# Optimization experiments

Measured on AMD Instinct MI355X. Metric: run time of the kernel, lower is better.

Reference implementation:

```python
import jax, jax.numpy as jnp
import numpy as np

N, D, DIN, S, R = 128, 2560, 5120, 16, 160  # users, d_model, d_inner, d_state, dt_rank


def setup_inputs() -> dict:
    key = jax.random.key(0)
    ks = jax.random.split(key, 16)
    f = lambda k, shape, s: jax.random.normal(k, shape, dtype=jnp.float32) * s
    return {
        "x": f(ks[0], (1, 1, N, D), 1.0),
        "conv_state0": f(ks[1], (1, 1, N, DIN), 0.1),
        "conv_state1": f(ks[2], (1, 1, N, DIN), 0.1),
        "conv_state2": f(ks[3], (1, 1, N, DIN), 0.1),
        "conv_state3": f(ks[4], (1, 1, N, DIN), 0.1),
        "ssm_state": f(ks[5], (N, DIN, S), 0.1),
        "ssm_proj": f(ks[6], (D, DIN), 0.02),
        "mlp_proj": f(ks[7], (D, DIN), 0.02),
        "down_proj": f(ks[8], (DIN, D), 0.02),
        "conv_w": f(ks[9], (4, DIN), 0.2),
        "conv_bias": f(ks[10], (DIN,), 0.1),
        "x_proj_w": f(ks[11], (DIN, R + 2 * S), 0.02),
        "dt_proj_w": f(ks[12], (R, DIN), 0.05),
        "dt_proj_b": f(ks[13], (DIN,), 0.1),
        "A_log": jnp.log(jnp.broadcast_to(jnp.arange(1, S + 1, dtype=jnp.float32), (DIN, S))),
        "D_param": jnp.ones((DIN,), jnp.float32),
    }


def reference(x, conv_state0, conv_state1, conv_state2, conv_state3, ssm_state,
              ssm_proj, mlp_proj, down_proj, conv_w, conv_bias,
              x_proj_w, dt_proj_w, dt_proj_b, A_log, D_param):
    r = dt_proj_w.shape[0]
    s = A_log.shape[1]
    x2 = x[0, 0]                         # (N, D)
    xs = x2 @ ssm_proj                   # (N, DIN) in_proj (ssm half)
    # shifted conv state window: oldest state (conv_state0) is dropped
    states = (conv_state1[0, 0], conv_state2[0, 0], conv_state3[0, 0], xs)
    conv_out = conv_bias + conv_w[0] * states[0] + conv_w[1] * states[1] \
        + conv_w[2] * states[2] + conv_w[3] * states[3]   # (N, DIN)
    u = jax.nn.silu(conv_out)
    # selective-scan single step (TtMambaSSM)
    proj = u @ x_proj_w                  # (N, R + 2S)
    dt = jax.nn.softplus(proj[:, :r] @ dt_proj_w + dt_proj_b)  # (N, DIN)
    Bm = proj[:, r:r + s]                # (N, S)
    Cm = proj[:, r + s:]                 # (N, S)
    A = -jnp.exp(A_log)                  # (DIN, S)
    dA = jnp.exp(dt[:, :, None] * A[None])                     # (N, DIN, S)
    h = dA * ssm_state + dt[:, :, None] * Bm[:, None, :] * u[:, :, None]
    y = jnp.einsum('nds,ns->nd', h, Cm) + D_param * u          # (N, DIN)
    # residual/gate branch and output projection (note: no silu on res, as in source)
    res = x2 @ mlp_proj                  # (N, DIN)
    out = (y * res) @ down_proj          # (N, D)
    return out[None, None]               # (1, 1, N, D)
```

## Files before the change

kernel.cpp:

```cpp
#include <hip/hip_runtime.h>

using u16 = unsigned short;
using u32 = unsigned int;

typedef __attribute__((ext_vector_type(8))) short short8;
typedef __attribute__((ext_vector_type(4))) float floatx4;

constexpr int TOKENS = 128;
constexpr int DM = 2560;
constexpr int DI = 5120;
constexpr int NS = 16;
constexpr int NR = 160;
constexpr int NP = 192;

constexpr size_t ND    = (size_t)TOKENS * DI;
constexpr size_t XS_P  = 0;
constexpr size_t RES_P = XS_P + 5 * ND;
constexpr size_t U_OFF = RES_P + 5 * ND;
constexpr size_t DT_P  = U_OFF + ND;
constexpr size_t PRJ_P = DT_P + 5 * ND;
constexpr size_t PRJ   = PRJ_P + 40 * (size_t)(TOKENS * NP);
constexpr size_t NEED  = PRJ + (size_t)(TOKENS * NP);

constexpr size_t S_XS  = 0;
constexpr size_t S_RES = S_XS + ND;
constexpr size_t S_U   = S_RES + ND;
constexpr size_t S_DT  = S_U + ND;
constexpr size_t S_PRJ = S_DT + ND;
constexpr size_t S_OAC = S_PRJ + (size_t)(TOKENS * NP);

__device__ __forceinline__ float bf2f(u16 h) {
  u32 u = ((u32)h) << 16;
  return __builtin_bit_cast(float, u);
}
__device__ __forceinline__ u16 f2bf(float f) {
  u32 u = __builtin_bit_cast(u32, f);
  u += 0x7FFFu + ((u >> 16) & 1u);
  return (u16)(u >> 16);
}
__device__ __forceinline__ u32 pk2(float a, float b) {
  u32 r;
  asm("v_cvt_pk_bf16_f32 %0, %1, %2" : "=v"(r) : "v"(a), "v"(b));
  return r;
}
__device__ __forceinline__ uint4 pack8(uint4 lo, uint4 hi) {
  float4 a = __builtin_bit_cast(float4, lo), b = __builtin_bit_cast(float4, hi);
  return (uint4){pk2(a.x, a.y), pk2(a.z, a.w), pk2(b.x, b.y), pk2(b.z, b.w)};
}
__device__ __forceinline__ float ldsc(const void* p, size_t i, bool bf) {
  return bf ? bf2f(((const u16*)p)[i]) : ((const float*)p)[i];
}
__device__ __forceinline__ void ld8f(const void* p, size_t i, bool bf, float* o) {
  if (bf) {
    uint4 v = *(const uint4*)((const u16*)p + i);
    const u16* h = (const u16*)&v;
#pragma unroll
    for (int e = 0; e < 8; e++) o[e] = bf2f(h[e]);
  } else {
    const float4* f = (const float4*)((const float*)p + i);
    float4 a = f[0], b = f[1];
    o[0] = a.x; o[1] = a.y; o[2] = a.z; o[3] = a.w;
    o[4] = b.x; o[5] = b.y; o[6] = b.z; o[7] = b.w;
  }
}

struct GemmP {
  const void* A; int lda; int a_ws;
  const void* B; const void* B2;
  float* C; float* C2;
  int ldb; int ldc;
  int ksteps;
  int nx_half;
  int atomic;
  size_t cstride;
  const u32* probe;
};

__global__ __launch_bounds__(256, 3) void gemm_k(GemmP p) {
  __shared__ __align__(16) u16 As[2 * 128 * 32];
  __shared__ __align__(16) u16 Bs[2 * 64 * 32];

  const bool bf = (p.probe[0] != 0u);
  const int tid = threadIdx.x;
  const int bx = blockIdx.x;
  const void* B = p.B; float* C = p.C;
  int nblk = bx;
  if (bx >= p.nx_half) { B = p.B2; C = p.C2; nblk = bx - p.nx_half; }
  const int n0 = nblk * 64;
  const int kstart = blockIdx.y * p.ksteps * 32;
  if (!p.atomic) C += blockIdx.y * p.cstride;

  const int wave = tid >> 6, lane = tid & 63;
  const int q = lane >> 4, l16 = lane & 15;
  const int wx = wave & 1, wy = wave >> 1;

  const bool a_f32 = p.a_ws || !bf;

  const int ac = tid & 3;
  const int am0 = tid >> 2;
  const bool bact = tid < 128;
  const int bc = tid & 7, pr = (tid >> 3) & 15;
  const int bn8 = bc * 8, k2 = 2 * pr;

  floatx4 acc[4][2];
#pragma unroll
  for (int mi = 0; mi < 4; mi++)
#pragma unroll
    for (int ni = 0; ni < 2; ni++) acc[mi][ni] = (floatx4){0.f, 0.f, 0.f, 0.f};

  auto load_tiles = [&](int ks, uint4* ra, uint4* rb) {
    const int kb = kstart + ks * 32;
    if (!a_f32) {
      ra[0] = *(const uint4*)((const u16*)p.A + (size_t)am0 * p.lda + kb + ac * 8);
      ra[1] = *(const uint4*)((const u16*)p.A + (size_t)(am0 + 64) * p.lda + kb + ac * 8);
    } else {
      const float* Af = (const float*)p.A;
      const float4* f0 = (const float4*)(Af + (size_t)am0 * p.lda + kb + ac * 8);
      const float4* f1 = (const float4*)(Af + (size_t)(am0 + 64) * p.lda + kb + ac * 8);
      ra[0] = __builtin_bit_cast(uint4, f0[0]); ra[1] = __builtin_bit_cast(uint4, f0[1]);
      ra[2] = __builtin_bit_cast(uint4, f1[0]); ra[3] = __builtin_bit_cast(uint4, f1[1]);
    }
    if (bact) {
      if (bf) {
        rb[0] = *(const uint4*)((const u16*)B + (size_t)(kb + k2) * p.ldb + n0 + bn8);
        rb[1] = *(const uint4*)((const u16*)B + (size_t)(kb + k2 + 1) * p.ldb + n0 + bn8);
      } else {
        const float* Bf = (const float*)B;
        const float4* g0 = (const float4*)(Bf + (size_t)(kb + k2) * p.ldb + n0 + bn8);
        const float4* g1 = (const float4*)(Bf + (size_t)(kb + k2 + 1) * p.ldb + n0 + bn8);
        rb[0] = __builtin_bit_cast(uint4, g0[0]); rb[1] = __builtin_bit_cast(uint4, g0[1]);
        rb[2] = __builtin_bit_cast(uint4, g1[0]); rb[3] = __builtin_bit_cast(uint4, g1[1]);
      }
    }
  };

  auto store_tiles = [&](int b, const uint4* ra, const uint4* rb) {
    u16* Ab = &As[b * 4096];
    u16* Bb = &Bs[b * 2048];
    uint4 w0, w1;
    if (!a_f32) { w0 = ra[0]; w1 = ra[1]; }
    else        { w0 = pack8(ra[0], ra[1]); w1 = pack8(ra[2], ra[3]); }
    *(uint4*)&Ab[am0 * 32 + ((ac ^ (am0 & 3)) << 3)] = w0;
    const int m1 = am0 + 64;
    *(uint4*)&Ab[m1 * 32 + ((ac ^ (m1 & 3)) << 3)] = w1;
    if (bact) {
      u32 pk[8];
      if (bf) {
        const u16* lo = (const u16*)&rb[0];
        const u16* hi = (const u16*)&rb[1];
#pragma unroll
        for (int j = 0; j < 8; j++) pk[j] = (u32)lo[j] | ((u32)hi[j] << 16);
      } else {
        const float* lo = (const float*)&rb[0];
        const float* hi = (const float*)&rb[2];
#pragma unroll
        for (int j = 0; j < 8; j++) pk[j] = pk2(lo[j], hi[j]);
      }
#pragma unroll
      for (int j = 0; j < 8; j++) {
        const int n = bn8 + j;
        const int blk = (k2 >> 3) ^ ((n ^ (n >> 3)) & 3);
        *(u32*)&Bb[n * 32 + (blk << 3) + (k2 & 7)] = pk[j];
      }
    }
  };

  const int swA = l16 & 3;
  const int arow = (wy * 64 + l16) * 32;
  const int ao = ((q ^ swA) << 3);
  int nrow[2], bo[2];
#pragma unroll
  for (int ni = 0; ni < 2; ni++) {
    const int n = wx * 32 + ni * 16 + l16;
    nrow[ni] = n * 32;
    bo[ni] = ((q ^ ((n ^ (n >> 3)) & 3)) << 3);
  }

  auto compute = [&](int b) {
    const u16* Ab = &As[b * 4096];
    const u16* Bb = &Bs[b * 2048];
    short8 a[4];
#pragma unroll
    for (int mi = 0; mi < 4; mi++)
      a[mi] = __builtin_bit_cast(short8, *(const uint4*)&Ab[arow + mi * 512 + ao]);
    short8 bb[2];
#pragma unroll
    for (int ni = 0; ni < 2; ni++)
      bb[ni] = __builtin_bit_cast(short8, *(const uint4*)&Bb[nrow[ni] + bo[ni]]);
#pragma unroll
    for (int mi = 0; mi < 4; mi++)
#pragma unroll
      for (int ni = 0; ni < 2; ni++)
        acc[mi][ni] = __builtin_amdgcn_mfma_f32_16x16x32_bf16(
            a[mi], bb[ni], acc[mi][ni], 0, 0, 0);
  };

#define FENCE_BAR()                                        \
  asm volatile("s_waitcnt lgkmcnt(0)" ::: "memory");       \
  __builtin_amdgcn_sched_barrier(0);                       \
  __builtin_amdgcn_s_barrier()

  uint4 ra0[4], rb0[4], ra1[4], rb1[4];
  load_tiles(0, ra0, rb0);
  if (p.ksteps > 1) load_tiles(1, ra1, rb1);
  int t = 0;
  for (;;) {
    store_tiles(0, ra0, rb0);
    if (t + 2 < p.ksteps) load_tiles(t + 2, ra0, rb0);
    FENCE_BAR();
    compute(0);
    if (++t == p.ksteps) break;

    store_tiles(1, ra1, rb1);
    if (t + 2 < p.ksteps) load_tiles(t + 2, ra1, rb1);
    FENCE_BAR();
    compute(1);
    if (++t == p.ksteps) break;
  }
#undef FENCE_BAR

#pragma unroll
  for (int ni = 0; ni < 2; ni++) {
    const int col = n0 + wx * 32 + ni * 16 + l16;
#pragma unroll
    for (int mi = 0; mi < 4; mi++) {
      floatx4 v = acc[mi][ni];
#pragma unroll
      for (int r = 0; r < 4; r++) {
        const int row = wy * 64 + mi * 16 + q * 4 + r;
        if (p.atomic) atomicAdd(&C[(size_t)row * p.ldc + col], v[r]);
        else          C[(size_t)row * p.ldc + col] = v[r];
      }
    }
  }
}

__global__ __launch_bounds__(256) void epi_u_k(
    const float* __restrict__ xs_p, int nred, size_t pstride,
    const void* __restrict__ cs1, const void* __restrict__ cs2,
    const void* __restrict__ cs3, const void* __restrict__ cw,
    const void* __restrict__ cb, float* __restrict__ u,
    const u32* __restrict__ probe) {
  const bool bf = (probe[0] != 0u);
  const int idx = blockIdx.x * 256 + threadIdx.x;
  const int n = idx / (DI / 8);
  const int d0 = (idx - n * (DI / 8)) * 8;
  const size_t nd = (size_t)n * DI + d0;
  float xv[8] = {0.f, 0.f, 0.f, 0.f, 0.f, 0.f, 0.f, 0.f};
  for (int j = 0; j < nred; j++) {
    const float4* f = (const float4*)(xs_p + j * pstride + nd);
    float4 a = f[0], b = f[1];
    xv[0] += a.x; xv[1] += a.y; xv[2] += a.z; xv[3] += a.w;
    xv[4] += b.x; xv[5] += b.y; xv[6] += b.z; xv[7] += b.w;
  }
  float c1[8], c2[8], c3[8], w0[8], w1[8], w2[8], w3[8], bb[8];
  ld8f(cs1, nd, bf, c1);
  ld8f(cs2, nd, bf, c2);
  ld8f(cs3, nd, bf, c3);
  ld8f(cw, (size_t)0 * DI + d0, bf, w0);
  ld8f(cw, (size_t)1 * DI + d0, bf, w1);
  ld8f(cw, (size_t)2 * DI + d0, bf, w2);
  ld8f(cw, (size_t)3 * DI + d0, bf, w3);
  ld8f(cb, d0, bf, bb);
  float o[8];
#pragma unroll
  for (int e = 0; e < 8; e++) {
    float cv = bb[e] + w0[e] * c1[e] + w1[e] * c2[e] + w2[e] * c3[e] +
               w3[e] * xv[e];
    o[e] = cv / (1.0f + __expf(-cv));
  }
  float4* uo = (float4*)(u + nd);
  uo[0] = (float4){o[0], o[1], o[2], o[3]};
  uo[1] = (float4){o[4], o[5], o[6], o[7]};
}

__global__ __launch_bounds__(256) void rproj_k(const float* __restrict__ in,
                                               int nred, size_t pstride,
                                               float* __restrict__ out) {
  const int i = blockIdx.x * 256 + threadIdx.x;
  if (i < TOKENS * NP) {
    float s = 0.f;
    for (int j = 0; j < nred; j++) s += in[j * pstride + i];
    out[i] = s;
  }
}

__global__ __launch_bounds__(256) void ssm_k(
    const void* __restrict__ sstate, const void* __restrict__ alog,
    const void* __restrict__ dparam, const void* __restrict__ dtb,
    const float* __restrict__ proj, const float* __restrict__ dt_p,
    int nred_d, size_t sd, const float* __restrict__ u,
    const float* __restrict__ res_p, int nred_r, size_t sr,
    float* __restrict__ z, const u32* __restrict__ probe) {
  const bool bf = (probe[0] != 0u);
  const int n = blockIdx.y;
  const int d = blockIdx.x * 256 + threadIdx.x;
  __shared__ float Bsh[NS], Csh[NS];
  if (threadIdx.x < NS)
    Bsh[threadIdx.x] = proj[(size_t)n * NP + NR + threadIdx.x];
  else if (threadIdx.x < 2 * NS)
    Csh[threadIdx.x - NS] = proj[(size_t)n * NP + NR + threadIdx.x];
  __syncthreads();
  const size_t nd = (size_t)n * DI + d;
  const float uv = u[nd];
  float rv = 0.f;
  for (int j = 0; j < nred_r; j++) rv += res_p[j * sr + nd];
  float sv = ldsc(dtb, d, bf);
  for (int j = 0; j < nred_d; j++) sv += dt_p[j * sd + nd];
  const float dtv = (sv > 20.0f) ? sv : log1pf(__expf(sv));

  float stf[16], alf[16];
  if (bf) {
    u16 st[16], al[16];
    const uint4* sp = (const uint4*)((const u16*)sstate + nd * 16);
    *(uint4*)&st[0] = sp[0]; *(uint4*)&st[8] = sp[1];
    const uint4* ap = (const uint4*)((const u16*)alog + (size_t)d * 16);
    *(uint4*)&al[0] = ap[0]; *(uint4*)&al[8] = ap[1];
#pragma unroll
    for (int s = 0; s < 16; s++) { stf[s] = bf2f(st[s]); alf[s] = bf2f(al[s]); }
  } else {
    const float4* sp = (const float4*)((const float*)sstate + nd * 16);
    const float4* ap = (const float4*)((const float*)alog + (size_t)d * 16);
#pragma unroll
    for (int i = 0; i < 4; i++) {
      float4 s4 = sp[i], a4 = ap[i];
      stf[i * 4 + 0] = s4.x; stf[i * 4 + 1] = s4.y; stf[i * 4 + 2] = s4.z; stf[i * 4 + 3] = s4.w;
      alf[i * 4 + 0] = a4.x; alf[i * 4 + 1] = a4.y; alf[i * 4 + 2] = a4.z; alf[i * 4 + 3] = a4.w;
    }
  }
  float y = 0.f;
#pragma unroll
  for (int s = 0; s < 16; s++) {
    float Aa = -__expf(alf[s]);
    float dA = __expf(dtv * Aa);
    float h = dA * stf[s] + dtv * Bsh[s] * uv;
    y += h * Csh[s];
  }
  y += ldsc(dparam, d, bf) * uv;
  z[nd] = y * rv;
}

__global__ __launch_bounds__(256) void cvt_k(const float* __restrict__ in,
                                             int nred, size_t pstride,
                                             void* __restrict__ out, int n,
                                             const u32* __restrict__ probe) {
  const bool bf = (probe[0] != 0u);
  const int i0 = (blockIdx.x * 256 + threadIdx.x) * 8;
  if (i0 + 8 <= n) {
    float o[8] = {0.f, 0.f, 0.f, 0.f, 0.f, 0.f, 0.f, 0.f};
    for (int j = 0; j < nred; j++) {
      const float4* f = (const float4*)(in + j * pstride + i0);
      float4 a = f[0], b = f[1];
      o[0] += a.x; o[1] += a.y; o[2] += a.z; o[3] += a.w;
      o[4] += b.x; o[5] += b.y; o[6] += b.z; o[7] += b.w;
    }
    if (bf) {
      uint4 v = {pk2(o[0], o[1]), pk2(o[2], o[3]), pk2(o[4], o[5]), pk2(o[6], o[7])};
      *(uint4*)((u16*)out + i0) = v;
    } else {
      float4* fo = (float4*)((float*)out + i0);
      fo[0] = (float4){o[0], o[1], o[2], o[3]};
      fo[1] = (float4){o[4], o[5], o[6], o[7]};
    }
  } else {
    for (int i = i0; i < n; i++) {
      float s = 0.f;
      for (int j = 0; j < nred; j++) s += in[j * pstride + i];
      if (bf) ((u16*)out)[i] = f2bf(s);
      else    ((float*)out)[i] = s;
    }
  }
}

extern "C" void kernel_launch(void* const* d_in, const int* in_sizes, int n_in,
                              void* d_out, int out_size, void* d_ws, size_t ws_size,
                              hipStream_t stream) {
  const void* x         = d_in[0];
  const void* cs1       = d_in[2];
  const void* cs2       = d_in[3];
  const void* cs3       = d_in[4];
  const void* ssm_state = d_in[5];
  const void* ssm_proj  = d_in[6];
  const void* mlp_proj  = d_in[7];
  const void* down_proj = d_in[8];
  const void* conv_w    = d_in[9];
  const void* conv_b    = d_in[10];
  const void* x_proj_w  = d_in[11];
  const void* dt_proj_w = d_in[12];
  const void* dt_proj_b = d_in[13];
  const void* A_log     = d_in[14];
  const void* D_param   = d_in[15];
  const u32*  probe     = (const u32*)A_log;

  float* ws = (float*)d_ws;
  const bool big = (ws_size / sizeof(float)) >= NEED;

  if (big) {
    float* xs_p  = ws + XS_P;
    float* res_p = ws + RES_P;
    float* u     = ws + U_OFF;
    float* dt_p  = ws + DT_P;
    float* prj_p = ws + PRJ_P;
    float* prj   = ws + PRJ;
    float* z     = ws + XS_P;
    float* oac_p = ws + RES_P;

    {
      GemmP p{};
      p.A = x; p.lda = DM; p.a_ws = 0;
      p.B = ssm_proj; p.B2 = mlp_proj;
      p.C = xs_p; p.C2 = res_p;
      p.ldb = DI; p.ldc = DI;
      p.ksteps = 16; p.nx_half = 80; p.atomic = 0; p.cstride = ND;
      p.probe = probe;
      gemm_k<<<dim3(160, 5), 256, 0, stream>>>(p);
    }
    epi_u_k<<<dim3(TOKENS * DI / 8 / 256), 256, 0, stream>>>(
        xs_p, 5, ND, cs1, cs2, cs3, conv_w, conv_b, u, probe);
    {
      GemmP p{};
      p.A = u; p.lda = DI; p.a_ws = 1;
      p.B = x_proj_w; p.B2 = nullptr;
      p.C = prj_p; p.C2 = nullptr;
      p.ldb = NP; p.ldc = NP;
      p.ksteps = 4; p.nx_half = 1 << 30; p.atomic = 0;
      p.cstride = (size_t)TOKENS * NP;
      p.probe = probe;
      gemm_k<<<dim3(3, 40), 256, 0, stream>>>(p);
    }
    rproj_k<<<dim3((TOKENS * NP + 255) / 256), 256, 0, stream>>>(
        prj_p, 40, (size_t)TOKENS * NP, prj);
    {
      GemmP p{};
      p.A = prj; p.lda = NP; p.a_ws = 1;
      p.B = dt_proj_w; p.B2 = nullptr;
      p.C = dt_p; p.C2 = nullptr;
      p.ldb = DI; p.ldc = DI;
      p.ksteps = 1; p.nx_half = 1 << 30; p.atomic = 0; p.cstride = ND;
      p.probe = probe;
      gemm_k<<<dim3(DI / 64, 5), 256, 0, stream>>>(p);
    }
    ssm_k<<<dim3(DI / 256, TOKENS), 256, 0, stream>>>(
        ssm_state, A_log, D_param, dt_proj_b, prj, dt_p, 5, ND, u,
        res_p, 5, ND, z, probe);
    {
      GemmP p{};
      p.A = z; p.lda = DI; p.a_ws = 1;
      p.B = down_proj; p.B2 = nullptr;
      p.C = oac_p; p.C2 = nullptr;
      p.ldb = DM; p.ldc = DM;
      p.ksteps = 16; p.nx_half = 1 << 30; p.atomic = 0;
      p.cstride = (size_t)TOKENS * DM;
      p.probe = probe;
      gemm_k<<<dim3(DM / 64, 10), 256, 0, stream>>>(p);
    }
    cvt_k<<<dim3((out_size / 8 + 255) / 256), 256, 0, stream>>>(
        oac_p, 10, (size_t)TOKENS * DM, d_out, out_size, probe);
  } else {
    float* xs  = ws + S_XS;
    float* res = ws + S_RES;
    float* u   = ws + S_U;
    float* dt  = ws + S_DT;
    float* prj = ws + S_PRJ;
    float* oac = ws + S_OAC;
    float* z   = ws + S_XS;

    hipMemsetAsync(xs,  0, ND * sizeof(float), stream);
    hipMemsetAsync(res, 0, ND * sizeof(float), stream);
    hipMemsetAsync(dt,  0, ND * sizeof(float), stream);
    hipMemsetAsync(prj, 0, (size_t)TOKENS * NP * sizeof(float), stream);
    hipMemsetAsync(oac, 0, (size_t)TOKENS * DM * sizeof(float), stream);

    {
      GemmP p{};
      p.A = x; p.lda = DM; p.a_ws = 0;
      p.B = ssm_proj; p.B2 = mlp_proj;
      p.C = xs; p.C2 = res;
      p.ldb = DI; p.ldc = DI;
      p.ksteps = 10; p.nx_half = 80; p.atomic = 1; p.cstride = 0;
      p.probe = probe;
      gemm_k<<<dim3(160, 8), 256, 0, stream>>>(p);
    }
    epi_u_k<<<dim3(TOKENS * DI / 8 / 256), 256, 0, stream>>>(
        xs, 1, 0, cs1, cs2, cs3, conv_w, conv_b, u, probe);
    {
      GemmP p{};
      p.A = u; p.lda = DI; p.a_ws = 1;
      p.B = x_proj_w; p.B2 = nullptr;
      p.C = prj; p.C2 = nullptr;
      p.ldb = NP; p.ldc = NP;
      p.ksteps = 4; p.nx_half = 1 << 30; p.atomic = 1; p.cstride = 0;
      p.probe = probe;
      gemm_k<<<dim3(3, 40), 256, 0, stream>>>(p);
    }
    {
      GemmP p{};
      p.A = prj; p.lda = NP; p.a_ws = 1;
      p.B = dt_proj_w; p.B2 = nullptr;
      p.C = dt; p.C2 = nullptr;
      p.ldb = DI; p.ldc = DI;
      p.ksteps = 1; p.nx_half = 1 << 30; p.atomic = 1; p.cstride = 0;
      p.probe = probe;
      gemm_k<<<dim3(DI / 64, 5), 256, 0, stream>>>(p);
    }
    ssm_k<<<dim3(DI / 256, TOKENS), 256, 0, stream>>>(
        ssm_state, A_log, D_param, dt_proj_b, prj, dt, 1, 0, u,
        res, 1, 0, z, probe);
    {
      GemmP p{};
      p.A = z; p.lda = DI; p.a_ws = 1;
      p.B = down_proj; p.B2 = nullptr;
      p.C = oac; p.C2 = nullptr;
      p.ldb = DM; p.ldc = DM;
      p.ksteps = 10; p.nx_half = 1 << 30; p.atomic = 1; p.cstride = 0;
      p.probe = probe;
      gemm_k<<<dim3(DM / 64, 16), 256, 0, stream>>>(p);
    }
    cvt_k<<<dim3((out_size / 8 + 255) / 256), 256, 0, stream>>>(
        oac, 1, 0, d_out, out_size, probe);
  }
}
```

Baseline: 314.3 us.

## Replace 256-thread shared-A GEMM with single-wave 64x32 tile GEMM

The 4-wave GEMM with a 128x64 tile, A and B staged in LDS and block barriers is replaced by a one-wave kernel. Each wave computes a 64x32 tile, reads A fragments straight from global memory into registers, stages only B in a small double-buffered LDS buffer, and needs no s_barrier. All launches now use a 3D grid (N, M, K-split), and the split-K partition counts and workspace sizes grow to match. The aim is more parallel blocks, no barrier stalls and less LDS traffic, at the cost of losing A reuse across waves and of larger split-K partial buffers and reductions.

```diff
diff --git a/kernel.cpp b/kernel.cpp
--- a/kernel.cpp
+++ b/kernel.cpp
@@ -15,11 +15,11 @@
 
 constexpr size_t ND    = (size_t)TOKENS * DI;
 constexpr size_t XS_P  = 0;
-constexpr size_t RES_P = XS_P + 5 * ND;
-constexpr size_t U_OFF = RES_P + 5 * ND;
+constexpr size_t RES_P = XS_P + 8 * ND;
+constexpr size_t U_OFF = RES_P + 8 * ND;
 constexpr size_t DT_P  = U_OFF + ND;
 constexpr size_t PRJ_P = DT_P + 5 * ND;
-constexpr size_t PRJ   = PRJ_P + 40 * (size_t)(TOKENS * NP);
+constexpr size_t PRJ   = PRJ_P + 80 * (size_t)(TOKENS * NP);
 constexpr size_t NEED  = PRJ + (size_t)(TOKENS * NP);
 
 constexpr size_t S_XS  = 0;
@@ -76,31 +76,24 @@
   const u32* probe;
 };
 
-__global__ __launch_bounds__(256, 3) void gemm_k(GemmP p) {
-  __shared__ __align__(16) u16 As[2 * 128 * 32];
-  __shared__ __align__(16) u16 Bs[2 * 64 * 32];
+__global__ __launch_bounds__(64, 4) void gemm_w(GemmP p) {
+  __shared__ __align__(16) u16 Bs[2 * 32 * 32];
 
   const bool bf = (p.probe[0] != 0u);
-  const int tid = threadIdx.x;
+  const int lane = threadIdx.x;
   const int bx = blockIdx.x;
   const void* B = p.B; float* C = p.C;
   int nblk = bx;
   if (bx >= p.nx_half) { B = p.B2; C = p.C2; nblk = bx - p.nx_half; }
-  const int n0 = nblk * 64;
-  const int kstart = blockIdx.y * p.ksteps * 32;
-  if (!p.atomic) C += blockIdx.y * p.cstride;
-
-  const int wave = tid >> 6, lane = tid & 63;
+  const int n0 = nblk * 32;
+  const int m0 = blockIdx.y * 64;
+  const int kstart = blockIdx.z * p.ksteps * 32;
+  if (!p.atomic) C += blockIdx.z * p.cstride;
+
+  const bool a_f32 = p.a_ws || !bf;
   const int q = lane >> 4, l16 = lane & 15;
-  const int wx = wave & 1, wy = wave >> 1;
-
-  const bool a_f32 = p.a_ws || !bf;
-
-  const int ac = tid & 3;
-  const int am0 = tid >> 2;
-  const bool bact = tid < 128;
-  const int bc = tid & 7, pr = (tid >> 3) & 15;
-  const int bn8 = bc * 8, k2 = 2 * pr;
+  const int k2 = 2 * (lane >> 2);
+  const int nseg = (lane & 3) * 8;
 
   floatx4 acc[4][2];
 #pragma unroll
@@ -108,42 +101,48 @@
 #pragma unroll
     for (int ni = 0; ni < 2; ni++) acc[mi][ni] = (floatx4){0.f, 0.f, 0.f, 0.f};
 
-  auto load_tiles = [&](int ks, uint4* ra, uint4* rb) {
-    const int kb = kstart + ks * 32;
+  uint4 ra[8], rb[4];
+
+  auto load_tiles = [&](int t) {
+    const int kb = kstart + t * 32;
     if (!a_f32) {
-      ra[0] = *(const uint4*)((const u16*)p.A + (size_t)am0 * p.lda + kb + ac * 8);
-      ra[1] = *(const uint4*)((const u16*)p.A + (size_t)(am0 + 64) * p.lda + kb + ac * 8);
+#pragma unroll
+      for (int mi = 0; mi < 4; mi++)
+        ra[mi] = *(const uint4*)((const u16*)p.A +
+                                 (size_t)(m0 + mi * 16 + l16) * p.lda + kb + q * 8);
     } else {
       const float* Af = (const float*)p.A;
-      const float4* f0 = (const float4*)(Af + (size_t)am0 * p.lda + kb + ac * 8);
-      const float4* f1 = (const float4*)(Af + (size_t)(am0 + 64) * p.lda + kb + ac * 8);
-      ra[0] = __builtin_bit_cast(uint4, f0[0]); ra[1] = __builtin_bit_cast(uint4, f0[1]);
-      ra[2] = __builtin_bit_cast(uint4, f1[0]); ra[3] = __builtin_bit_cast(uint4, f1[1]);
-    }
-    if (bact) {
-      if (bf) {
-        rb[0] = *(const uint4*)((const u16*)B + (size_t)(kb + k2) * p.ldb + n0 + bn8);
-        rb[1] = *(const uint4*)((const u16*)B + (size_t)(kb + k2 + 1) * p.ldb + n0 + bn8);
-      } else {
-        const float* Bf = (const float*)B;
-        const float4* g0 = (const float4*)(Bf + (size_t)(kb + k2) * p.ldb + n0 + bn8);
-        const float4* g1 = (const float4*)(Bf + (size_t)(kb + k2 + 1) * p.ldb + n0 + bn8);
-        rb[0] = __builtin_bit_cast(uint4, g0[0]); rb[1] = __builtin_bit_cast(uint4, g0[1]);
-        rb[2] = __builtin_bit_cast(uint4, g1[0]); rb[3] = __builtin_bit_cast(uint4, g1[1]);
+#pragma unroll
+      for (int mi = 0; mi < 4; mi++) {
+        const float4* f = (const float4*)(Af + (size_t)(m0 + mi * 16 + l16) * p.lda + kb + q * 8);
+        ra[2 * mi] = __builtin_bit_cast(uint4, f[0]);
+        ra[2 * mi + 1] = __builtin_bit_cast(uint4, f[1]);
       }
     }
+    if (bf) {
+      rb[0] = *(const uint4*)((const u16*)B + (size_t)(kb + k2) * p.ldb + n0 + nseg);
+      rb[1] = *(const uint4*)((const u16*)B + (size_t)(kb + k2 + 1) * p.ldb + n0 + nseg);
+    } else {
+      const float* Bf = (const float*)B;
+      const float4* g0 = (const float4*)(Bf + (size_t)(kb + k2) * p.ldb + n0 + nseg);
+      const float4* g1 = (const float4*)(Bf + (size_t)(kb + k2 + 1) * p.ldb + n0 + nseg);
+      rb[0] = __builtin_bit_cast(uint4, g0[0]); rb[1] = __builtin_bit_cast(uint4, g0[1]);
+      rb[2] = __builtin_bit_cast(uint4, g1[0]); rb[3] = __builtin_bit_cast(uint4, g1[1]);
+    }
   };
 
-  auto store_tiles = [&](int b, const uint4* ra, const uint4* rb) {
-    u16* Ab = &As[b * 4096];
-    u16* Bb = &Bs[b * 2048];
-    uint4 w0, w1;
-    if (!a_f32) { w0 = ra[0]; w1 = ra[1]; }
-    else        { w0 = pack8(ra[0], ra[1]); w1 = pack8(ra[2], ra[3]); }
-    *(uint4*)&Ab[am0 * 32 + ((ac ^ (am0 & 3)) << 3)] = w0;
-    const int m1 = am0 + 64;
-    *(uint4*)&Ab[m1 * 32 + ((ac ^ (m1 & 3)) << 3)] = w1;
-    if (bact) {
+  int boff[2];
+#pragma unroll
+  for (int ni = 0; ni < 2; ni++) {
+    const int n = ni * 16 + l16;
+    boff[ni] = n * 32 + ((q ^ ((n ^ (n >> 3)) & 3)) << 3);
+  }
+
+  load_tiles(0);
+  int c = 0;
+  for (int t = 0;;) {
+    u16* Bb = &Bs[c * 1024];
+    {
       u32 pk[8];
       if (bf) {
         const u16* lo = (const u16*)&rb[0];
@@ -158,76 +157,52 @@
       }
 #pragma unroll
       for (int j = 0; j < 8; j++) {
-        const int n = bn8 + j;
+        const int n = nseg + j;
         const int blk = (k2 >> 3) ^ ((n ^ (n >> 3)) & 3);
         *(u32*)&Bb[n * 32 + (blk << 3) + (k2 & 7)] = pk[j];
       }
     }
-  };
-
-  const int swA = l16 & 3;
-  const int arow = (wy * 64 + l16) * 32;
-  const int ao = ((q ^ swA) << 3);
-  int nrow[2], bo[2];
-#pragma unroll
-  for (int ni = 0; ni < 2; ni++) {
-    const int n = wx * 32 + ni * 16 + l16;
-    nrow[ni] = n * 32;
-    bo[ni] = ((q ^ ((n ^ (n >> 3)) & 3)) << 3);
-  }
-
-  auto compute = [&](int b) {
-    const u16* Ab = &As[b * 4096];
-    const u16* Bb = &Bs[b * 2048];
-    short8 a[4];
-#pragma unroll
-    for (int mi = 0; mi < 4; mi++)
-      a[mi] = __builtin_bit_cast(short8, *(const uint4*)&Ab[arow + mi * 512 + ao]);
-    short8 bb[2];
+    short8 af[4];
+    if (!a_f32) {
+#pragma unroll
+      for (int mi = 0; mi < 4; mi++) af[mi] = __builtin_bit_cast(short8, ra[mi]);
+    } else {
+#pragma unroll
+      for (int mi = 0; mi < 4; mi++)
+        af[mi] = __builtin_bit_cast(short8, pack8(ra[2 * mi], ra[2 * mi + 1]));
+    }
+
+    asm volatile("s_waitcnt lgkmcnt(0)" ::: "memory");
+    __builtin_amdgcn_sched_barrier(0);
+
+    short8 bfr[2];
 #pragma unroll
     for (int ni = 0; ni < 2; ni++)
-      bb[ni] = __builtin_bit_cast(short8, *(const uint4*)&Bb[nrow[ni] + bo[ni]]);
+      bfr[ni] = __builtin_bit_cast(short8, *(const uint4*)&Bb[boff[ni]]);
+
+    const bool more = (t + 1 < p.ksteps);
+    if (more) load_tiles(t + 1);
+
 #pragma unroll
     for (int mi = 0; mi < 4; mi++)
 #pragma unroll
       for (int ni = 0; ni < 2; ni++)
         acc[mi][ni] = __builtin_amdgcn_mfma_f32_16x16x32_bf16(
-            a[mi], bb[ni], acc[mi][ni], 0, 0, 0);
-  };
-
-#define FENCE_BAR()                                        \
-  asm volatile("s_waitcnt lgkmcnt(0)" ::: "memory");       \
-  __builtin_amdgcn_sched_barrier(0);                       \
-  __builtin_amdgcn_s_barrier()
-
-  uint4 ra0[4], rb0[4], ra1[4], rb1[4];
-  load_tiles(0, ra0, rb0);
-  if (p.ksteps > 1) load_tiles(1, ra1, rb1);
-  int t = 0;
-  for (;;) {
-    store_tiles(0, ra0, rb0);
-    if (t + 2 < p.ksteps) load_tiles(t + 2, ra0, rb0);
-    FENCE_BAR();
-    compute(0);
-    if (++t == p.ksteps) break;
-
-    store_tiles(1, ra1, rb1);
-    if (t + 2 < p.ksteps) load_tiles(t + 2, ra1, rb1);
-    FENCE_BAR();
-    compute(1);
-    if (++t == p.ksteps) break;
-  }
-#undef FENCE_BAR
+            af[mi], bfr[ni], acc[mi][ni], 0, 0, 0);
+
+    if (!more) break;
+    ++t; c ^= 1;
+  }
 
 #pragma unroll
   for (int ni = 0; ni < 2; ni++) {
-    const int col = n0 + wx * 32 + ni * 16 + l16;
+    const int col = n0 + ni * 16 + l16;
 #pragma unroll
     for (int mi = 0; mi < 4; mi++) {
       floatx4 v = acc[mi][ni];
 #pragma unroll
       for (int r = 0; r < 4; r++) {
-        const int row = wy * 64 + mi * 16 + q * 4 + r;
+        const int row = m0 + mi * 16 + q * 4 + r;
         if (p.atomic) atomicAdd(&C[(size_t)row * p.ldc + col], v[r]);
         else          C[(size_t)row * p.ldc + col] = v[r];
       }
@@ -411,25 +386,25 @@
       p.B = ssm_proj; p.B2 = mlp_proj;
       p.C = xs_p; p.C2 = res_p;
       p.ldb = DI; p.ldc = DI;
-      p.ksteps = 16; p.nx_half = 80; p.atomic = 0; p.cstride = ND;
-      p.probe = probe;
-      gemm_k<<<dim3(160, 5), 256, 0, stream>>>(p);
+      p.ksteps = 10; p.nx_half = 160; p.atomic = 0; p.cstride = ND;
+      p.probe = probe;
+      gemm_w<<<dim3(320, 2, 8), 64, 0, stream>>>(p);
     }
     epi_u_k<<<dim3(TOKENS * DI / 8 / 256), 256, 0, stream>>>(
-        xs_p, 5, ND, cs1, cs2, cs3, conv_w, conv_b, u, probe);
+        xs_p, 8, ND, cs1, cs2, cs3, conv_w, conv_b, u, probe);
     {
       GemmP p{};
       p.A = u; p.lda = DI; p.a_ws = 1;
       p.B = x_proj_w; p.B2 = nullptr;
       p.C = prj_p; p.C2 = nullptr;
       p.ldb = NP; p.ldc = NP;
-      p.ksteps = 4; p.nx_half = 1 << 30; p.atomic = 0;
+      p.ksteps = 2; p.nx_half = 1 << 30; p.atomic = 0;
       p.cstride = (size_t)TOKENS * NP;
       p.probe = probe;
-      gemm_k<<<dim3(3, 40), 256, 0, stream>>>(p);
+      gemm_w<<<dim3(6, 2, 80), 64, 0, stream>>>(p);
     }
     rproj_k<<<dim3((TOKENS * NP + 255) / 256), 256, 0, stream>>>(
-        prj_p, 40, (size_t)TOKENS * NP, prj);
+        prj_p, 80, (size_t)TOKENS * NP, prj);
     {
       GemmP p{};
       p.A = prj; p.lda = NP; p.a_ws = 1;
@@ -438,24 +413,24 @@
       p.ldb = DI; p.ldc = DI;
       p.ksteps = 1; p.nx_half = 1 << 30; p.atomic = 0; p.cstride = ND;
       p.probe = probe;
-      gemm_k<<<dim3(DI / 64, 5), 256, 0, stream>>>(p);
+      gemm_w<<<dim3(160, 2, 5), 64, 0, stream>>>(p);
     }
     ssm_k<<<dim3(DI / 256, TOKENS), 256, 0, stream>>>(
         ssm_state, A_log, D_param, dt_proj_b, prj, dt_p, 5, ND, u,
-        res_p, 5, ND, z, probe);
+        res_p, 8, ND, z, probe);
     {
       GemmP p{};
       p.A = z; p.lda = DI; p.a_ws = 1;
       p.B = down_proj; p.B2 = nullptr;
       p.C = oac_p; p.C2 = nullptr;
       p.ldb = DM; p.ldc = DM;
-      p.ksteps = 16; p.nx_half = 1 << 30; p.atomic = 0;
+      p.ksteps = 10; p.nx_half = 1 << 30; p.atomic = 0;
       p.cstride = (size_t)TOKENS * DM;
       p.probe = probe;
-      gemm_k<<<dim3(DM / 64, 10), 256, 0, stream>>>(p);
+      gemm_w<<<dim3(80, 2, 16), 64, 0, stream>>>(p);
     }
     cvt_k<<<dim3((out_size / 8 + 255) / 256), 256, 0, stream>>>(
-        oac_p, 10, (size_t)TOKENS * DM, d_out, out_size, probe);
+        oac_p, 16, (size_t)TOKENS * DM, d_out, out_size, probe);
   } else {
     float* xs  = ws + S_XS;
     float* res = ws + S_RES;
@@ -477,9 +452,9 @@
       p.B = ssm_proj; p.B2 = mlp_proj;
       p.C = xs; p.C2 = res;
       p.ldb = DI; p.ldc = DI;
-      p.ksteps = 10; p.nx_half = 80; p.atomic = 1; p.cstride = 0;
-      p.probe = probe;
-      gemm_k<<<dim3(160, 8), 256, 0, stream>>>(p);
+      p.ksteps = 10; p.nx_half = 160; p.atomic = 1; p.cstride = 0;
+      p.probe = probe;
+      gemm_w<<<dim3(320, 2, 8), 64, 0, stream>>>(p);
     }
     epi_u_k<<<dim3(TOKENS * DI / 8 / 256), 256, 0, stream>>>(
         xs, 1, 0, cs1, cs2, cs3, conv_w, conv_b, u, probe);
@@ -489,9 +464,9 @@
       p.B = x_proj_w; p.B2 = nullptr;
       p.C = prj; p.C2 = nullptr;
       p.ldb = NP; p.ldc = NP;
-      p.ksteps = 4; p.nx_half = 1 << 30; p.atomic = 1; p.cstride = 0;
-      p.probe = probe;
-      gemm_k<<<dim3(3, 40), 256, 0, stream>>>(p);
+      p.ksteps = 2; p.nx_half = 1 << 30; p.atomic = 1; p.cstride = 0;
+      p.probe = probe;
+      gemm_w<<<dim3(6, 2, 80), 64, 0, stream>>>(p);
     }
     {
       GemmP p{};
@@ -501,7 +476,7 @@
       p.ldb = DI; p.ldc = DI;
       p.ksteps = 1; p.nx_half = 1 << 30; p.atomic = 1; p.cstride = 0;
       p.probe = probe;
-      gemm_k<<<dim3(DI / 64, 5), 256, 0, stream>>>(p);
+      gemm_w<<<dim3(160, 2, 5), 64, 0, stream>>>(p);
     }
     ssm_k<<<dim3(DI / 256, TOKENS), 256, 0, stream>>>(
         ssm_state, A_log, D_param, dt_proj_b, prj, dt, 1, 0, u,
@@ -514,7 +489,7 @@
       p.ldb = DM; p.ldc = DM;
       p.ksteps = 10; p.nx_half = 1 << 30; p.atomic = 1; p.cstride = 0;
       p.probe = probe;
-      gemm_k<<<dim3(DM / 64, 16), 256, 0, stream>>>(p);
+      gemm_w<<<dim3(80, 2, 16), 64, 0, stream>>>(p);
     }
     cvt_k<<<dim3((out_size / 8 + 255) / 256), 256, 0, stream>>>(
         oac, 1, 0, d_out, out_size, probe);
```

Measured after the change: 376.6 us. 1.2x slower.
